# Kernel tuning notes

Hardware: AMD Instinct MI355X
Metric: run time of the kernel (lower is better)

Reference implementation:

```python
import jax, jax.numpy as jnp
import numpy as np

B, L, F = 4, 8192, 1024
H, D = 16, 64
EPS = 1e-6

def _phi(x):
    # ELU+1 positive feature map, standard for linear attention
    return jax.nn.elu(x) + 1.0

def setup_inputs() -> dict:
    key = jax.random.key(0)
    ks = jax.random.split(key, 6)
    s_in = 1.0
    s_w = 1.0 / np.sqrt(F)
    s_o = 1.0 / np.sqrt(H * D)
    return {
        "inputs_q": jax.random.normal(ks[0], (B, L, F), jnp.float32),
        "inputs_kv": jax.random.normal(ks[1], (B, L, F), jnp.float32),
        "Wq": jax.random.normal(ks[2], (F, H, D), jnp.float32) * s_w,
        "Wk": jax.random.normal(ks[3], (F, H, D), jnp.float32) * s_w,
        "Wv": jax.random.normal(ks[4], (F, H, D), jnp.float32) * s_w,
        "Wo": jax.random.normal(ks[5], (H, D, F), jnp.float32) * s_o,
    }

def reference(inputs_q, inputs_kv, Wq, Wk, Wv, Wo):
    # QKV projections (split-head kernels, no bias)
    q = jnp.einsum('bqf,fhd->bqhd', inputs_q, Wq)   # [B,Lq,H,D]
    k = jnp.einsum('bkf,fhd->bkhd', inputs_kv, Wk)  # [B,Lk,H,D]
    v = jnp.einsum('bkf,fhd->bkhd', inputs_kv, Wv)  # [B,Lk,H,D]

    qp = _phi(q)
    kp = _phi(k)

    # Linear attention: O = phi(q) @ (phi(k)^T V) / (phi(q) . sum_k phi(k))
    kv = jnp.einsum('bkhd,bkhe->bhde', kp, v)       # [B,H,D,D] small state
    ksum = jnp.sum(kp, axis=1)                       # [B,H,D]
    z = 1.0 / (jnp.einsum('bqhd,bhd->bqh', qp, ksum) + EPS)
    out = jnp.einsum('bqhd,bhde,bqh->bqhe', qp, kv, z)  # [B,Lq,H,D]

    # Output projection
    return jnp.einsum('bqhe,hef->bqf', out, Wo)      # [B,Lq,F]
```

## Files before the change

kernel.cpp:

```cpp
#include <hip/hip_runtime.h>
#include <hip/hip_fp16.h>
#include <math.h>

typedef _Float16 half8  __attribute__((ext_vector_type(8)));
typedef _Float16 half4v __attribute__((ext_vector_type(4)));
typedef float    floatx4 __attribute__((ext_vector_type(4)));

#define NB   4
#define LL   8192
#define FF   1024
#define HH   16
#define DD   64
#define MTOT 32768
#define KK   1024
#define NN   1024
#define ZSCALE 65536.0f

__device__ __forceinline__ void gload_lds16(const void* g, void* l) {
  __builtin_amdgcn_global_load_lds(
      (const __attribute__((address_space(1))) void*)g,
      (__attribute__((address_space(3))) void*)l, 16, 0, 0);
}

__device__ __forceinline__ float phi_act(float x) {
  return x > 0.f ? x + 1.f : __expf(x);
}

__global__ void k_cvt(const float* __restrict__ src, _Float16* __restrict__ dst, int n4) {
  int stride = gridDim.x * blockDim.x;
  for (int i = blockIdx.x * blockDim.x + threadIdx.x; i < n4; i += stride) {
    float4 v = reinterpret_cast<const float4*>(src)[i];
    half4v h;
    h[0] = (_Float16)v.x; h[1] = (_Float16)v.y; h[2] = (_Float16)v.z; h[3] = (_Float16)v.w;
    reinterpret_cast<half4v*>(dst)[i] = h;
  }
}

__global__ void k_cvt_t(const float* __restrict__ W0, const float* __restrict__ W1,
                        const float* __restrict__ W2,
                        _Float16* __restrict__ T0, _Float16* __restrict__ T1,
                        _Float16* __restrict__ T2) {
  __shared__ float tile[32][33];
  int bid = blockIdx.x;
  int w = bid >> 10, rem = bid & 1023;
  int ti = rem >> 5, tj = rem & 31;
  const float* src = (w == 0) ? W0 : (w == 1) ? W1 : W2;
  _Float16*    dst = (w == 0) ? T0 : (w == 1) ? T1 : T2;
  int t = threadIdx.x;
  int r = t >> 3, c4 = (t & 7) << 2;
  float4 v = *reinterpret_cast<const float4*>(&src[(size_t)(ti * 32 + r) * FF + tj * 32 + c4]);
  tile[r][c4 + 0] = v.x; tile[r][c4 + 1] = v.y; tile[r][c4 + 2] = v.z; tile[r][c4 + 3] = v.w;
  __syncthreads();
  half4v h;
  h[0] = (_Float16)tile[c4 + 0][r];
  h[1] = (_Float16)tile[c4 + 1][r];
  h[2] = (_Float16)tile[c4 + 2][r];
  h[3] = (_Float16)tile[c4 + 3][r];
  *reinterpret_cast<half4v*>(&dst[(size_t)(tj * 32 + r) * FF + ti * 32 + c4]) = h;
}


template<int MATB, int HALF>
__device__ __forceinline__ void stage_half(const _Float16* __restrict__ G, int row0,
                                           int col0, _Float16* plane, int tid) {
  #pragma unroll
  for (int is = 0; is < 2; ++is) {
    int lin = is * 8192 + tid * 16;
    int swz = lin ^ (((lin >> 7) & 7) << 4);
    int rp = swz >> 7;
    int kb = swz & 127;
    int row;
    if constexpr (MATB) row = (rp >> 5) * 64 + HALF * 32 + (rp & 31);
    else                row = (rp >> 6) * 128 + HALF * 64 + (rp & 63);
    gload_lds16(G + (size_t)(row0 + row) * 1024 + col0 + (kb >> 1),
                (char*)plane + lin);
  }
}

__device__ __forceinline__ half8 frag_read(const _Float16* plane, int rp, int kk, int lh) {
  int byte = rp * 128 + kk * 64 + lh * 16;
  byte ^= ((byte >> 7) & 7) << 4;
  return *(const half8*)((const char*)plane + byte);
}

template<int MH, int NH>
__device__ __forceinline__ void qreads(const _Float16* sm, int buf,
                                       half8 (&bA)[8], half8 (&bB)[2][4],
                                       int wr, int wc, int lr, int lh) {
  if constexpr (NH == 0) {
    const _Float16* Ap = sm + buf * 32768 + MH * 8192;
    #pragma unroll
    for (int m = 0; m < 4; ++m)
      #pragma unroll
      for (int kk = 0; kk < 2; ++kk)
        bA[m * 2 + kk] = frag_read(Ap, wr * 64 + m * 16 + lr, kk, lh);
  }
  if constexpr (MH == 0) {
    const _Float16* Bp = sm + buf * 32768 + 16384 + NH * 8192;
    #pragma unroll
    for (int n = 0; n < 2; ++n)
      #pragma unroll
      for (int kk = 0; kk < 2; ++kk)
        bB[NH][n * 2 + kk] = frag_read(Bp, wc * 32 + n * 16 + lr, kk, lh);
  }
}

template<int MH, int NH, bool VM4>
__device__ __forceinline__ void qmfma(half8 (&bA)[8], half8 (&bB)[2][4],
                                      floatx4 (&acc)[8][4]) {
  if constexpr (VM4) {
    asm volatile("s_waitcnt vmcnt(4)" ::: "memory");
  }
  __builtin_amdgcn_s_barrier();
  asm volatile("s_waitcnt lgkmcnt(0)" ::: "memory");
  __builtin_amdgcn_sched_barrier(0);
  __builtin_amdgcn_s_setprio(1);
  #pragma unroll
  for (int m = 0; m < 4; ++m)
    #pragma unroll
    for (int n = 0; n < 2; ++n)
      #pragma unroll
      for (int kk = 0; kk < 2; ++kk)
        acc[MH * 4 + m][NH * 2 + n] = __builtin_amdgcn_mfma_f32_16x16x32_f16(
            bA[m * 2 + kk], bB[NH][n * 2 + kk], acc[MH * 4 + m][NH * 2 + n], 0, 0, 0);
  __builtin_amdgcn_s_setprio(0);
  __builtin_amdgcn_s_barrier();
}

template<int TBUF>
__device__ __forceinline__ void do_tile(int t, const _Float16* __restrict__ Ab,
                                        const _Float16* __restrict__ Bb,
                                        int i0, int j0, _Float16* sm, int tid,
                                        half8 (&bA)[8], half8 (&bB)[2][4],
                                        floatx4 (&acc)[8][4],
                                        int wr, int wc, int lr, int lh) {
  _Float16* self  = sm + TBUF * 32768;
  _Float16* other = sm + (TBUF ^ 1) * 32768;
  const int c1 = ((t + 1 < 16) ? (t + 1) : 15) * 64;
  const int c2 = ((t + 2 < 16) ? (t + 2) : 15) * 64;
  qreads<0, 0>(sm, TBUF, bA, bB, wr, wc, lr, lh);
  stage_half<1, 1>(Bb, j0, c1, other + 24576, tid);
  qmfma<0, 0, false>(bA, bB, acc);
  qreads<0, 1>(sm, TBUF, bA, bB, wr, wc, lr, lh);
  stage_half<0, 1>(Ab, i0, c1, other + 8192, tid);
  qmfma<0, 1, false>(bA, bB, acc);
  qreads<1, 0>(sm, TBUF, bA, bB, wr, wc, lr, lh);
  stage_half<0, 0>(Ab, i0, c2, self + 0, tid);
  qmfma<1, 0, false>(bA, bB, acc);
  stage_half<1, 0>(Bb, j0, c2, self + 16384, tid);
  qmfma<1, 1, true>(bA, bB, acc);
}

template<int MODE, bool PHI>
__global__ __launch_bounds__(512, 2)
void k_gemm(const _Float16* __restrict__ A, const _Float16* __restrict__ BT,
            void* __restrict__ Cptr, float outScale) {
  __shared__ __align__(16) _Float16 smem[65536];
  const int tid  = threadIdx.x;
  const int lane = tid & 63;
  const int wid  = tid >> 6;
  const int wr = wid >> 2, wc = wid & 3;
  const int lr = lane & 15, lh = lane >> 4;

  const int tile = (blockIdx.x & 7) * 64 + (blockIdx.x >> 3);
  const int tm = tile >> 2, tn = tile & 3;
  const int i0 = tm * 256, j0 = tn * 256;

  const _Float16* Ab = A;
  const _Float16* Bb = (MODE == 2) ? BT + ((size_t)(i0 >> 13)) * ((size_t)NN * KK) : BT;

  floatx4 acc[8][4];
  #pragma unroll
  for (int m = 0; m < 8; ++m)
    #pragma unroll
    for (int n = 0; n < 4; ++n)
      #pragma unroll
      for (int r = 0; r < 4; ++r) acc[m][n][r] = 0.f;

  _Float16* sm = (_Float16*)smem;
  half8 bA[8];
  half8 bB[2][4];

  stage_half<0, 0>(Ab, i0, 0,  sm + 0,             tid);
  stage_half<1, 0>(Bb, j0, 0,  sm + 16384,         tid);
  stage_half<1, 1>(Bb, j0, 0,  sm + 24576,         tid);
  stage_half<0, 1>(Ab, i0, 0,  sm + 8192,          tid);
  stage_half<0, 0>(Ab, i0, 64, sm + 32768 + 0,     tid);
  stage_half<1, 0>(Bb, j0, 64, sm + 32768 + 16384, tid);
  asm volatile("s_waitcnt vmcnt(4)" ::: "memory");
  __builtin_amdgcn_s_barrier();

  #pragma unroll 1
  for (int tt = 0; tt < 8; ++tt) {
    do_tile<0>(2 * tt,     Ab, Bb, i0, j0, sm, tid, bA, bB, acc, wr, wc, lr, lh);
    do_tile<1>(2 * tt + 1, Ab, Bb, i0, j0, sm, tid, bA, bB, acc, wr, wc, lr, lh);
  }

  asm volatile("s_waitcnt vmcnt(0)" ::: "memory");
  __builtin_amdgcn_s_barrier();

  if constexpr (MODE == 0) {
    _Float16* C = (_Float16*)Cptr;
    #pragma unroll
    for (int m = 0; m < 8; ++m) {
      int row = i0 + wr * 128 + m * 16 + lh * 4;
      #pragma unroll
      for (int n = 0; n < 4; ++n) {
        int col = j0 + wc * 64 + n * 16 + lr;
        #pragma unroll
        for (int r = 0; r < 4; ++r) {
          float v = acc[m][n][r];
          if constexpr (PHI) v = phi_act(v);
          C[(size_t)(row + r) * NN + col] = (_Float16)v;
        }
      }
    }
  } else if constexpr (MODE == 2) {
    float* C = (float*)Cptr;
    #pragma unroll
    for (int m = 0; m < 8; ++m) {
      int row = i0 + wr * 128 + m * 16 + lh * 4;
      #pragma unroll
      for (int n = 0; n < 4; ++n) {
        int col = j0 + wc * 64 + n * 16 + lr;
        #pragma unroll
        for (int r = 0; r < 4; ++r)
          C[(size_t)(row + r) * NN + col] = acc[m][n][r] * outScale;
      }
    }
  } else {
    #pragma unroll
    for (int m = 0; m < 8; ++m) {
      int l0l = wr * 128 + m * 16 + lh * 4;
      #pragma unroll
      for (int n = 0; n < 4; ++n) {
        int n_loc = wc * 64 + n * 16 + lr;
        int byte = (n_loc * 512 + l0l * 2) ^ ((n_loc & 7) << 4);
        half4v h;
        #pragma unroll
        for (int r = 0; r < 4; ++r) {
          float v = acc[m][n][r];
          if constexpr (PHI) v = phi_act(v);
          h[r] = (_Float16)v;
        }
        *(half4v*)((char*)sm + byte) = h;
      }
    }
    __syncthreads();
    _Float16* C = (_Float16*)Cptr;
    const int bb = i0 >> 13;
    const int l0 = i0 & 8191;
    #pragma unroll 1
    for (int pass = 0; pass < 16; ++pass) {
      int n_loc = pass * 16 + (tid >> 5);
      int lo = (tid & 31) * 16;
      int byte = (n_loc * 512 + lo) ^ ((n_loc & 7) << 4);
      half8 v = *(const half8*)((char*)sm + byte);
      *(half8*)&C[((size_t)bb * 1024 + j0 + n_loc) * LL + l0 + (lo >> 1)] = v;
    }
  }
}

__global__ void k_ksum(const _Float16* __restrict__ kpT, float* __restrict__ ksum) {
  int w = threadIdx.x >> 6, lane = threadIdx.x & 63;
  int row = blockIdx.x * 4 + w;
  const _Float16* p = kpT + (size_t)row * LL;
  float s = 0.f;
  for (int j = 0; j < 16; ++j) {
    half8 v = *(const half8*)&p[j * 512 + lane * 8];
    #pragma unroll
    for (int e = 0; e < 8; ++e) s += (float)v[e];
  }
  #pragma unroll
  for (int off = 1; off < 64; off <<= 1) s += __shfl_xor(s, off);
  if (lane == 0) ksum[row] = s;
}

__global__ __launch_bounds__(64)
void k_stageB(const _Float16* __restrict__ kpT, const _Float16* __restrict__ vT,
              float* __restrict__ kvpart) {
  __shared__ _Float16 Ak[64 * 72];
  __shared__ _Float16 Bv[64 * 72];
  const int bid = blockIdx.x;
  const int bh = bid >> 4, cc = bid & 15;
  const int lane = threadIdx.x;
  const int lr = lane & 15, lh = lane >> 4;
  const _Float16* Ab = kpT + (size_t)bh * 64 * LL + cc * 512;
  const _Float16* Bb = vT  + (size_t)bh * 64 * LL + cc * 512;

  floatx4 acc[4][4];
  #pragma unroll
  for (int m = 0; m < 4; ++m)
    #pragma unroll
    for (int n = 0; n < 4; ++n)
      #pragma unroll
      for (int r = 0; r < 4; ++r) acc[m][n][r] = 0.f;

  for (int kt = 0; kt < 512; kt += 64) {
    __syncthreads();
    #pragma unroll
    for (int j = 0; j < 8; ++j) {
      int chunk = lane + 64 * j;
      int rr = chunk >> 3;
      int off = (chunk & 7) * 8;
      *(half8*)&Ak[rr * 72 + off] = *(const half8*)&Ab[(size_t)rr * LL + kt + off];
      *(half8*)&Bv[rr * 72 + off] = *(const half8*)&Bb[(size_t)rr * LL + kt + off];
    }
    __syncthreads();
    #pragma unroll
    for (int ks = 0; ks < 2; ++ks) {
      half8 af[4], bf[4];
      #pragma unroll
      for (int m = 0; m < 4; ++m) af[m] = *(const half8*)&Ak[(m * 16 + lr) * 72 + ks * 32 + lh * 8];
      #pragma unroll
      for (int n = 0; n < 4; ++n) bf[n] = *(const half8*)&Bv[(n * 16 + lr) * 72 + ks * 32 + lh * 8];
      #pragma unroll
      for (int m = 0; m < 4; ++m)
        #pragma unroll
        for (int n = 0; n < 4; ++n)
          acc[m][n] = __builtin_amdgcn_mfma_f32_16x16x32_f16(af[m], bf[n], acc[m][n], 0, 0, 0);
    }
  }
  float* op = kvpart + (size_t)bid * 4096;
  #pragma unroll
  for (int m = 0; m < 4; ++m)
    #pragma unroll
    for (int n = 0; n < 4; ++n)
      #pragma unroll
      for (int r = 0; r < 4; ++r)
        op[(m * 16 + lh * 4 + r) * 64 + n * 16 + lr] = acc[m][n][r];
}

__global__ void k_reduce_kv(const float* __restrict__ kvpart, float* __restrict__ kv) {
  int gid = blockIdx.x * 256 + threadIdx.x;
  int bh = gid >> 12, i = gid & 4095;
  float s = 0.f;
  for (int c = 0; c < 16; ++c) s += kvpart[((size_t)bh * 16 + c) * 4096 + i];
  kv[gid] = s;
}

__global__ void k_zscale(_Float16* __restrict__ qp, const float* __restrict__ ksum) {
  int w = threadIdx.x >> 6, lane = threadIdx.x & 63;
  int row = blockIdx.x * 4 + w;
  int b = row >> 13;
  int h = lane >> 2;
  _Float16* p = qp + (size_t)row * 1024 + lane * 16;
  half8 v0 = *(half8*)&p[0];
  half8 v1 = *(half8*)&p[8];
  const float* ks = ksum + ((size_t)b * 16 + h) * 64 + (lane & 3) * 16;
  float dot = 0.f;
  #pragma unroll
  for (int e = 0; e < 8; ++e) dot += (float)v0[e] * ks[e];
  #pragma unroll
  for (int e = 0; e < 8; ++e) dot += (float)v1[e] * ks[8 + e];
  dot += __shfl_xor(dot, 1);
  dot += __shfl_xor(dot, 2);
  float zf = ZSCALE / (dot + 1e-6f);
  #pragma unroll
  for (int e = 0; e < 8; ++e) v0[e] = (_Float16)((float)v0[e] * zf);
  #pragma unroll
  for (int e = 0; e < 8; ++e) v1[e] = (_Float16)((float)v1[e] * zf);
  *(half8*)&p[0] = v0;
  *(half8*)&p[8] = v1;
}

__global__ __launch_bounds__(256)
void k_mker(const float* __restrict__ kv, const _Float16* __restrict__ Wo16,
            _Float16* __restrict__ MT) {
  __shared__ float kvs[4096];
  int bid = blockIdx.x;
  int fc = bid & 3, h = (bid >> 2) & 15, b = bid >> 6;
  const float* kvp = kv + ((size_t)b * 16 + h) * 4096;
  for (int i = threadIdx.x; i < 4096; i += 256) kvs[i] = kvp[i];
  __syncthreads();
  int f = fc * 256 + threadIdx.x;
  float acc[64];
  #pragma unroll
  for (int d = 0; d < 64; ++d) acc[d] = 0.f;
  for (int e = 0; e < 64; ++e) {
    float wv = (float)Wo16[(size_t)(h * 64 + e) * 1024 + f];
    #pragma unroll
    for (int d = 0; d < 64; ++d) acc[d] = fmaf(kvs[d * 64 + e], wv, acc[d]);
  }
  _Float16* op = MT + ((size_t)b * 1024 + f) * 1024 + h * 64;
  #pragma unroll
  for (int g = 0; g < 8; ++g) {
    half8 o;
    #pragma unroll
    for (int j = 0; j < 8; ++j) o[j] = (_Float16)acc[g * 8 + j];
    *(half8*)&op[g * 8] = o;
  }
}

extern "C" void kernel_launch(void* const* d_in, const int* in_sizes, int n_in,
                              void* d_out, int out_size, void* d_ws, size_t ws_size,
                              hipStream_t stream) {
  (void)in_sizes; (void)n_in; (void)out_size; (void)ws_size;
  const float* xq  = (const float*)d_in[0];
  const float* xkv = (const float*)d_in[1];
  const float* Wq  = (const float*)d_in[2];
  const float* Wk  = (const float*)d_in[3];
  const float* Wv  = (const float*)d_in[4];
  const float* Wo  = (const float*)d_in[5];

  char* ws = (char*)d_ws;
  _Float16* qp16 = (_Float16*)(ws + 0);
  _Float16* kpT  = (_Float16*)(ws + 67108864);
  _Float16* vT   = (_Float16*)(ws + 134217728);
  _Float16* WqT  = (_Float16*)(ws + 201326592);
  _Float16* WkT  = (_Float16*)(ws + 203423744);
  _Float16* WvT  = (_Float16*)(ws + 205520896);
  _Float16* Wo16 = (_Float16*)(ws + 207618048);
  float*    ksum = (float*)(ws + 209715200);
  float*    kv   = (float*)(ws + 209731584);
  float*    kvpart = (float*)(ws + 210780160);
  _Float16* MT   = (_Float16*)(ws + 227557376);

  _Float16* Xq16  = (_Float16*)d_out;
  _Float16* Xkv16 = Xq16 + 33554432;

  k_cvt<<<2048, 256, 0, stream>>>(xq,  Xq16,  8388608);
  k_cvt<<<2048, 256, 0, stream>>>(xkv, Xkv16, 8388608);
  k_cvt<<<512,  256, 0, stream>>>(Wo,  Wo16,  262144);
  k_cvt_t<<<3072, 256, 0, stream>>>(Wq, Wk, Wv, WqT, WkT, WvT);

  k_gemm<0, true ><<<512, 512, 0, stream>>>(Xq16,  WqT, qp16, 1.0f);
  k_gemm<1, true ><<<512, 512, 0, stream>>>(Xkv16, WkT, kpT,  1.0f);
  k_gemm<1, false><<<512, 512, 0, stream>>>(Xkv16, WvT, vT,   1.0f);

  k_ksum<<<1024, 256, 0, stream>>>(kpT, ksum);
  k_stageB<<<1024, 64, 0, stream>>>(kpT, vT, kvpart);
  k_reduce_kv<<<1024, 256, 0, stream>>>(kvpart, kv);

  k_zscale<<<8192, 256, 0, stream>>>(qp16, ksum);

  k_mker<<<256, 256, 0, stream>>>(kv, Wo16, MT);
  k_gemm<2, false><<<512, 512, 0, stream>>>(qp16, MT, d_out, 1.0f / ZSCALE);
}
```

Baseline: 515.9 us.

## Merge K and V projection GEMMs and fuse key-sum into epilogue

The K and V projections now run as one GEMM launch over a doubled N dimension. This relies on WkT/WvT and kpT/vT sitting contiguously in the workspace, and the tile mapping is adjusted to cover the wider output. The phi activation and per-column partial sums for ksum are computed in the epilogue for the K half only. The old ksum kernel, which re-read the whole kpT buffer, is replaced by a small reduction over the partial sums. It also drops the explicit lgkmcnt wait and sched_barrier before the MFMA block, leaving the compiler to place LDS waits, which may change instruction scheduling.

```diff
diff --git a/kernel.cpp b/kernel.cpp
--- a/kernel.cpp
+++ b/kernel.cpp
@@ -112,8 +112,6 @@
     asm volatile("s_waitcnt vmcnt(4)" ::: "memory");
   }
   __builtin_amdgcn_s_barrier();
-  asm volatile("s_waitcnt lgkmcnt(0)" ::: "memory");
-  __builtin_amdgcn_sched_barrier(0);
   __builtin_amdgcn_s_setprio(1);
   #pragma unroll
   for (int m = 0; m < 4; ++m)
@@ -154,7 +152,7 @@
 template<int MODE, bool PHI>
 __global__ __launch_bounds__(512, 2)
 void k_gemm(const _Float16* __restrict__ A, const _Float16* __restrict__ BT,
-            void* __restrict__ Cptr, float outScale) {
+            void* __restrict__ Cptr, float* __restrict__ aux, float outScale) {
   __shared__ __align__(16) _Float16 smem[65536];
   const int tid  = threadIdx.x;
   const int lane = tid & 63;
@@ -162,8 +160,10 @@
   const int wr = wid >> 2, wc = wid & 3;
   const int lr = lane & 15, lh = lane >> 4;
 
-  const int tile = (blockIdx.x & 7) * 64 + (blockIdx.x >> 3);
-  const int tm = tile >> 2, tn = tile & 3;
+  constexpr int NT = (MODE == 1) ? 8 : 4;
+  constexpr int CH = (MODE == 1) ? 128 : 64;
+  const int tile = (blockIdx.x & 7) * CH + (blockIdx.x >> 3);
+  const int tm = tile / NT, tn = tile % NT;
   const int i0 = tm * 256, j0 = tn * 256;
 
   const _Float16* Ab = A;
@@ -229,6 +229,11 @@
       }
     }
   } else {
+    const int seg = j0 >> 10;
+    const int j0s = j0 & 1023;
+    const int bb  = i0 >> 13;
+    const int l0  = i0 & 8191;
+    float s[4] = {0.f, 0.f, 0.f, 0.f};
     #pragma unroll
     for (int m = 0; m < 8; ++m) {
       int l0l = wr * 128 + m * 16 + lh * 4;
@@ -240,40 +245,45 @@
         #pragma unroll
         for (int r = 0; r < 4; ++r) {
           float v = acc[m][n][r];
-          if constexpr (PHI) v = phi_act(v);
+          if (seg == 0) { v = phi_act(v); s[n] += v; }
           h[r] = (_Float16)v;
         }
         *(half4v*)((char*)sm + byte) = h;
       }
     }
+    if (seg == 0) {
+      #pragma unroll
+      for (int n = 0; n < 4; ++n) {
+        s[n] += __shfl_xor(s[n], 16);
+        s[n] += __shfl_xor(s[n], 32);
+      }
+      if (lh == 0) {
+        int ch = (l0 >> 7) + wr;
+        size_t base = ((size_t)bb * 64 + ch) * 1024 + j0s + wc * 64 + lr;
+        #pragma unroll
+        for (int n = 0; n < 4; ++n) aux[base + n * 16] = s[n];
+      }
+    }
     __syncthreads();
     _Float16* C = (_Float16*)Cptr;
-    const int bb = i0 >> 13;
-    const int l0 = i0 & 8191;
+    const size_t nbase = ((size_t)seg * 4 + bb) * 1024 + j0s;
     #pragma unroll 1
     for (int pass = 0; pass < 16; ++pass) {
       int n_loc = pass * 16 + (tid >> 5);
       int lo = (tid & 31) * 16;
       int byte = (n_loc * 512 + lo) ^ ((n_loc & 7) << 4);
       half8 v = *(const half8*)((char*)sm + byte);
-      *(half8*)&C[((size_t)bb * 1024 + j0 + n_loc) * LL + l0 + (lo >> 1)] = v;
-    }
-  }
-}
-
-__global__ void k_ksum(const _Float16* __restrict__ kpT, float* __restrict__ ksum) {
-  int w = threadIdx.x >> 6, lane = threadIdx.x & 63;
-  int row = blockIdx.x * 4 + w;
-  const _Float16* p = kpT + (size_t)row * LL;
+      *(half8*)&C[(nbase + n_loc) * LL + l0 + (lo >> 1)] = v;
+    }
+  }
+}
+
+__global__ void k_ksum_red(const float* __restrict__ part, float* __restrict__ ksum) {
+  int i = blockIdx.x * 256 + threadIdx.x;
+  int b = i >> 10, col = i & 1023;
   float s = 0.f;
-  for (int j = 0; j < 16; ++j) {
-    half8 v = *(const half8*)&p[j * 512 + lane * 8];
-    #pragma unroll
-    for (int e = 0; e < 8; ++e) s += (float)v[e];
-  }
-  #pragma unroll
-  for (int off = 1; off < 64; off <<= 1) s += __shfl_xor(s, off);
-  if (lane == 0) ksum[row] = s;
+  for (int c = 0; c < 64; ++c) s += part[((size_t)b * 64 + c) * 1024 + col];
+  ksum[i] = s;
 }
 
 __global__ __launch_bounds__(64)
@@ -414,6 +424,7 @@
   float*    ksum = (float*)(ws + 209715200);
   float*    kv   = (float*)(ws + 209731584);
   float*    kvpart = (float*)(ws + 210780160);
+  float*    ksum_part = (float*)(ws + 210780160);
   _Float16* MT   = (_Float16*)(ws + 227557376);
 
   _Float16* Xq16  = (_Float16*)d_out;
@@ -424,16 +435,15 @@
   k_cvt<<<512,  256, 0, stream>>>(Wo,  Wo16,  262144);
   k_cvt_t<<<3072, 256, 0, stream>>>(Wq, Wk, Wv, WqT, WkT, WvT);
 
-  k_gemm<0, true ><<<512, 512, 0, stream>>>(Xq16,  WqT, qp16, 1.0f);
-  k_gemm<1, true ><<<512, 512, 0, stream>>>(Xkv16, WkT, kpT,  1.0f);
-  k_gemm<1, false><<<512, 512, 0, stream>>>(Xkv16, WvT, vT,   1.0f);
-
-  k_ksum<<<1024, 256, 0, stream>>>(kpT, ksum);
+  k_gemm<0, true ><<<512,  512, 0, stream>>>(Xq16,  WqT, qp16, nullptr,   1.0f);
+  k_gemm<1, false><<<1024, 512, 0, stream>>>(Xkv16, WkT, kpT,  ksum_part, 1.0f);
+
+  k_ksum_red<<<16, 256, 0, stream>>>(ksum_part, ksum);
   k_stageB<<<1024, 64, 0, stream>>>(kpT, vT, kvpart);
   k_reduce_kv<<<1024, 256, 0, stream>>>(kvpart, kv);
 
   k_zscale<<<8192, 256, 0, stream>>>(qp16, ksum);
 
   k_mker<<<256, 256, 0, stream>>>(kv, Wo16, MT);
-  k_gemm<2, false><<<512, 512, 0, stream>>>(qp16, MT, d_out, 1.0f / ZSCALE);
-}
+  k_gemm<2, false><<<512, 512, 0, stream>>>(qp16, MT, d_out, nullptr, 1.0f / ZSCALE);
+}
```

New measurement: 502.6 us. 1.03x faster.
